# Performance work log

Measured on AMD Instinct MI355X. Metric: run time of the kernel, lower is better.

The kernel has to match this reference:

```python
import jax, jax.numpy as jnp
import numpy as np

N_VOCAB = 50400
D_MODEL = 4096
SHARDS = 8
SEQ = 2048
BATCH = 2
PER_IN = N_VOCAB // SHARDS      # 6300 vocab rows per shard
PER_OUT = D_MODEL // SHARDS     # 512 pos-emb dims per shard


def setup_inputs() -> dict:
    key = jax.random.key(0)
    k1, k2, k3, k4 = jax.random.split(key, 4)
    x = jax.random.randint(k1, (BATCH, SEQ), 0, N_VOCAB, dtype=jnp.int32)
    # Dense kernel [n_vocab, d_model] (vocab-sharded in the original) and bias [d_model]
    kernel = jax.random.truncated_normal(k2, -2.0, 2.0, (N_VOCAB, D_MODEL), dtype=jnp.float32) / np.sqrt(N_VOCAB)
    bias = jnp.zeros((D_MODEL,), dtype=jnp.float32)
    # per-shard positional embeddings, stacked as the all_gather result [shards, seq, per_out]
    pos_embs = 0.02 * jax.random.truncated_normal(k3, -2.0, 2.0, (SHARDS, SEQ, PER_OUT), dtype=jnp.float32)
    return {"x": x, "kernel": kernel, "bias": bias, "pos_embs": pos_embs}


def reference(x, kernel, bias, pos_embs):
    # Each shard s computes one_hot(clip(x - s*PER_IN, 0, PER_IN-1)) @ kernel_s + bias,
    # then psum over shards. Equivalent math via clipped gather into the full kernel:
    starts = jnp.arange(SHARDS, dtype=x.dtype) * PER_IN                 # [S]
    local = jnp.clip(x[None, :, :] - starts[:, None, None], 0, PER_IN - 1)
    gidx = local + starts[:, None, None]                                 # [S, B, T] global rows
    emb = kernel[gidx].sum(axis=0)                                       # [B, T, D] psum over shards
    emb = emb + jnp.asarray(SHARDS, bias.dtype) * bias                   # bias summed by psum S times
    # all_gather(pos_embs) -> [S, seq, per_out]; reshape(seq, -1) as in the original
    all_pos = pos_embs.reshape(SEQ, -1)                                  # [seq, d_model]
    return emb + all_pos[None, :, :]                                     # [B, T, D]
```

## Files before the change

kernel.cpp:

```cpp
#include <hip/hip_runtime.h>

#define N_VOCAB 50400
#define D_MODEL 4096
#define SHARDS  8
#define SEQ     2048
#define BATCH   2
#define PER_IN  6300

typedef float f4 __attribute__((ext_vector_type(4)));

__global__ __launch_bounds__(256)
void boundary_sums_kernel(const float* __restrict__ kern,
                          const float* __restrict__ bias,
                          float* __restrict__ bsum) {
    const int s  = blockIdx.x >> 2;
    const int c  = blockIdx.x & 3;
    const int d4 = c * 256 + threadIdx.x;

    const f4* __restrict__ kf = (const f4*)kern;
    const f4* __restrict__ bf = (const f4*)bias;

    f4 acc = (float)SHARDS * bf[d4];
#pragma unroll
    for (int sp = 0; sp < SHARDS; ++sp) {
        if (sp < s)
            acc += kf[(size_t)(sp * PER_IN + PER_IN - 1) * (D_MODEL / 4) + d4];
        else if (sp > s)
            acc += kf[(size_t)(sp * PER_IN) * (D_MODEL / 4) + d4];
    }
    ((f4*)bsum)[(size_t)s * (D_MODEL / 4) + d4] = acc;
}

__global__ __launch_bounds__(256)
void embed_gather_kernel(const int* __restrict__ x,
                         const float* __restrict__ kern,
                         const float* __restrict__ pos,
                         const float* __restrict__ bsum,
                         float* __restrict__ out) {
    const int t    = blockIdx.x >> 1;
    const int half = blockIdx.x & 1;
    const int tid  = threadIdx.x;
    const int base = half * (D_MODEL / 8);

    const int row0 = x[t];
    const int row1 = x[SEQ + t];
    const int s0 = row0 / PER_IN;
    const int s1 = row1 / PER_IN;

    const f4* __restrict__ k0 = (const f4*)(kern + (size_t)row0 * D_MODEL) + base;
    const f4* __restrict__ k1 = (const f4*)(kern + (size_t)row1 * D_MODEL) + base;
    const f4* __restrict__ pr = (const f4*)(pos  + (size_t)t    * D_MODEL) + base;
    const f4* __restrict__ b0 = (const f4*)(bsum + (size_t)s0   * D_MODEL) + base;
    const f4* __restrict__ b1 = (const f4*)(bsum + (size_t)s1   * D_MODEL) + base;
    f4* __restrict__ o0 = (f4*)(out + (size_t)t         * D_MODEL) + base;
    f4* __restrict__ o1 = (f4*)(out + (size_t)(SEQ + t) * D_MODEL) + base;

    f4 a0[2], a1[2], pv[2], v0[2], v1[2];
#pragma unroll
    for (int k = 0; k < 2; ++k) {
        const int i = tid + k * 256;
        a0[k] = __builtin_nontemporal_load(&k0[i]);
        a1[k] = __builtin_nontemporal_load(&k1[i]);
        pv[k] = __builtin_nontemporal_load(&pr[i]);
        v0[k] = b0[i];
        v1[k] = b1[i];
    }
#pragma unroll
    for (int k = 0; k < 2; ++k) {
        const int i = tid + k * 256;
        f4 r0 = a0[k] + v0[k] + pv[k];
        f4 r1 = a1[k] + v1[k] + pv[k];
        __builtin_nontemporal_store(r0, &o0[i]);
        __builtin_nontemporal_store(r1, &o1[i]);
    }
}

extern "C" void kernel_launch(void* const* d_in, const int* in_sizes, int n_in,
                              void* d_out, int out_size, void* d_ws, size_t ws_size,
                              hipStream_t stream) {
    const int*   x    = (const int*)  d_in[0];
    const float* kern = (const float*)d_in[1];
    const float* bias = (const float*)d_in[2];
    const float* pos  = (const float*)d_in[3];

    float* out  = (float*)d_out;
    float* bsum = (float*)d_ws;

    boundary_sums_kernel<<<SHARDS * (D_MODEL / 4 / 256), 256, 0, stream>>>(kern, bias, bsum);

    embed_gather_kernel<<<SEQ * 2, 256, 0, stream>>>(x, kern, pos, bsum, out);
}
```

Baseline: 37.68 us.

## Fuse boundary-row sums into the gather kernel and drop the precompute launch

Removes the separate boundary_sums kernel and its workspace round-trip. Each gather block now recomputes the sum of the seven clipped boundary rows per token directly from the kernel matrix, plus the scaled bias. This saves one launch and the serialization between the two kernels. In exchange, every block issues up to 14 extra row loads, served mostly from cache since only 16 distinct boundary rows exist, and the non-temporal load hints are dropped.

```diff
diff --git a/kernel.cpp b/kernel.cpp
--- a/kernel.cpp
+++ b/kernel.cpp
@@ -10,33 +10,11 @@
 typedef float f4 __attribute__((ext_vector_type(4)));
 
 __global__ __launch_bounds__(256)
-void boundary_sums_kernel(const float* __restrict__ kern,
-                          const float* __restrict__ bias,
-                          float* __restrict__ bsum) {
-    const int s  = blockIdx.x >> 2;
-    const int c  = blockIdx.x & 3;
-    const int d4 = c * 256 + threadIdx.x;
-
-    const f4* __restrict__ kf = (const f4*)kern;
-    const f4* __restrict__ bf = (const f4*)bias;
-
-    f4 acc = (float)SHARDS * bf[d4];
-#pragma unroll
-    for (int sp = 0; sp < SHARDS; ++sp) {
-        if (sp < s)
-            acc += kf[(size_t)(sp * PER_IN + PER_IN - 1) * (D_MODEL / 4) + d4];
-        else if (sp > s)
-            acc += kf[(size_t)(sp * PER_IN) * (D_MODEL / 4) + d4];
-    }
-    ((f4*)bsum)[(size_t)s * (D_MODEL / 4) + d4] = acc;
-}
-
-__global__ __launch_bounds__(256)
-void embed_gather_kernel(const int* __restrict__ x,
-                         const float* __restrict__ kern,
-                         const float* __restrict__ pos,
-                         const float* __restrict__ bsum,
-                         float* __restrict__ out) {
+void fused_embed_kernel(const int* __restrict__ x,
+                        const float* __restrict__ kern,
+                        const float* __restrict__ bias,
+                        const float* __restrict__ pos,
+                        float* __restrict__ out) {
     const int t    = blockIdx.x >> 1;
     const int half = blockIdx.x & 1;
     const int tid  = threadIdx.x;
@@ -50,29 +28,46 @@
     const f4* __restrict__ k0 = (const f4*)(kern + (size_t)row0 * D_MODEL) + base;
     const f4* __restrict__ k1 = (const f4*)(kern + (size_t)row1 * D_MODEL) + base;
     const f4* __restrict__ pr = (const f4*)(pos  + (size_t)t    * D_MODEL) + base;
-    const f4* __restrict__ b0 = (const f4*)(bsum + (size_t)s0   * D_MODEL) + base;
-    const f4* __restrict__ b1 = (const f4*)(bsum + (size_t)s1   * D_MODEL) + base;
+    const f4* __restrict__ bi = (const f4*)bias + base;
     f4* __restrict__ o0 = (f4*)(out + (size_t)t         * D_MODEL) + base;
     f4* __restrict__ o1 = (f4*)(out + (size_t)(SEQ + t) * D_MODEL) + base;
 
-    f4 a0[2], a1[2], pv[2], v0[2], v1[2];
+    const int i0 = tid;
+    const int i1 = tid + 256;
+
+    f4 a00 = k0[i0], a01 = k0[i1];
+    f4 a10 = k1[i0], a11 = k1[i1];
+    f4 p0  = pr[i0], p1  = pr[i1];
+    f4 bv0 = bi[i0], bv1 = bi[i1];
+
+    f4 acc00 = {0.f, 0.f, 0.f, 0.f}, acc01 = acc00;
+    f4 acc10 = acc00, acc11 = acc00;
 #pragma unroll
-    for (int k = 0; k < 2; ++k) {
-        const int i = tid + k * 256;
-        a0[k] = __builtin_nontemporal_load(&k0[i]);
-        a1[k] = __builtin_nontemporal_load(&k1[i]);
-        pv[k] = __builtin_nontemporal_load(&pr[i]);
-        v0[k] = b0[i];
-        v1[k] = b1[i];
+    for (int sp = 0; sp < SHARDS; ++sp) {
+        if (sp != s0) {
+            const size_t r = (size_t)(sp * PER_IN + (sp < s0 ? PER_IN - 1 : 0));
+            const f4* __restrict__ p = (const f4*)(kern + r * D_MODEL) + base;
+            acc00 += p[i0];
+            acc01 += p[i1];
+        }
+        if (sp != s1) {
+            const size_t r = (size_t)(sp * PER_IN + (sp < s1 ? PER_IN - 1 : 0));
+            const f4* __restrict__ p = (const f4*)(kern + r * D_MODEL) + base;
+            acc10 += p[i0];
+            acc11 += p[i1];
+        }
     }
-#pragma unroll
-    for (int k = 0; k < 2; ++k) {
-        const int i = tid + k * 256;
-        f4 r0 = a0[k] + v0[k] + pv[k];
-        f4 r1 = a1[k] + v1[k] + pv[k];
-        __builtin_nontemporal_store(r0, &o0[i]);
-        __builtin_nontemporal_store(r1, &o1[i]);
-    }
+
+    const float bs = (float)SHARDS;
+    f4 r00 = a00 + acc00 + bs * bv0 + p0;
+    f4 r01 = a01 + acc01 + bs * bv1 + p1;
+    f4 r10 = a10 + acc10 + bs * bv0 + p0;
+    f4 r11 = a11 + acc11 + bs * bv1 + p1;
+
+    __builtin_nontemporal_store(r00, &o0[i0]);
+    __builtin_nontemporal_store(r01, &o0[i1]);
+    __builtin_nontemporal_store(r10, &o1[i0]);
+    __builtin_nontemporal_store(r11, &o1[i1]);
 }
 
 extern "C" void kernel_launch(void* const* d_in, const int* in_sizes, int n_in,
@@ -83,10 +78,7 @@
     const float* bias = (const float*)d_in[2];
     const float* pos  = (const float*)d_in[3];
 
-    float* out  = (float*)d_out;
-    float* bsum = (float*)d_ws;
+    float* out = (float*)d_out;
 
-    boundary_sums_kernel<<<SHARDS * (D_MODEL / 4 / 256), 256, 0, stream>>>(kern, bias, bsum);
-
-    embed_gather_kernel<<<SEQ * 2, 256, 0, stream>>>(x, kern, pos, bsum, out);
+    fused_embed_kernel<<<SEQ * 2, 256, 0, stream>>>(x, kern, bias, pos, out);
 }
```

Result: faster. 36.05 us (-4.3%).
